# Performance work log

Hardware: AMD Instinct MI355X
Metric: run time of the kernel (lower is better)

## Reference

```python
import jax, jax.numpy as jnp
import numpy as np

N_NODES = 100000
N_EDGES = 1600000
IN_DIM = 128
HID = 64
N_CLASSES = 40
NEG_SLOPE = 0.2


def setup_inputs() -> dict:
    key = jax.random.key(0)
    ks = jax.random.split(key, 12)
    s_in = 1.0 / np.sqrt(IN_DIM)
    s_h = 1.0 / np.sqrt(HID)
    return {
        "x": jax.random.normal(ks[0], (N_NODES, IN_DIM), dtype=jnp.float32),
        "edge_index": jax.random.randint(ks[1], (2, N_EDGES), 0, N_NODES, dtype=jnp.int64),
        "W0": jax.random.normal(ks[2], (IN_DIM, HID), dtype=jnp.float32) * s_in,
        "a_s0": jax.random.normal(ks[3], (HID,), dtype=jnp.float32) * s_h,
        "a_d0": jax.random.normal(ks[4], (HID,), dtype=jnp.float32) * s_h,
        "b0": jnp.zeros((HID,), dtype=jnp.float32),
        "W1": jax.random.normal(ks[5], (HID, HID), dtype=jnp.float32) * s_h,
        "a_s1": jax.random.normal(ks[6], (HID,), dtype=jnp.float32) * s_h,
        "a_d1": jax.random.normal(ks[7], (HID,), dtype=jnp.float32) * s_h,
        "b1": jnp.zeros((HID,), dtype=jnp.float32),
        "Wl": jax.random.normal(ks[8], (HID, N_CLASSES), dtype=jnp.float32) * s_h,
        "bl": jnp.zeros((N_CLASSES,), dtype=jnp.float32),
    }


def gat_conv(x, src, dst, W, a_s, a_d, b, n_nodes):
    # single-head GATConv (PyG default heads=1), self-loops already in src/dst
    h = x @ W                                  # [N, d]
    e = jax.nn.leaky_relu((h @ a_s)[src] + (h @ a_d)[dst], NEG_SLOPE)  # [E]
    # segment softmax over incoming edges of each dst node
    m = jax.ops.segment_max(e, dst, num_segments=n_nodes)
    p = jnp.exp(e - m[dst])
    denom = jax.ops.segment_sum(p, dst, num_segments=n_nodes)
    alpha = p / (denom[dst] + 1e-16)           # [E]
    out = jax.ops.segment_sum(alpha[:, None] * h[src], dst, num_segments=n_nodes)
    return out + b


def reference(x, edge_index, W0, a_s0, a_d0, b0, W1, a_s1, a_d1, b1, Wl, bl):
    n = x.shape[0]
    loop = jnp.arange(n, dtype=edge_index.dtype)
    src = jnp.concatenate([edge_index[0], loop])
    dst = jnp.concatenate([edge_index[1], loop])
    h = gat_conv(x, src, dst, W0, a_s0, a_d0, b0, n)
    h = jax.nn.elu(h)
    h = gat_conv(h, src, dst, W1, a_s1, a_d1, b1, n)
    h = jax.nn.elu(h)
    return h @ Wl + bl
```

## Files before the change

### kernel.cpp

```cpp
#include <hip/hip_runtime.h>
#include <math.h>

#define NEG_SLOPE 0.2f
#define CAP 256
#define BSH 9
#define BSZ 512
#define CHUNK 4096
#define PADS 16
#define CAPQ 16384
#define CAPB 10240

typedef __attribute__((ext_vector_type(8))) short short8;
typedef __attribute__((ext_vector_type(4))) float f32x4;

__device__ __forceinline__ float hred_sum(float v) {
#pragma unroll
    for (int o = 16; o >= 1; o >>= 1) v += __shfl_xor(v, o, 64);
    return v;
}
__device__ __forceinline__ unsigned int f2bf(float f) {
    unsigned int u = __float_as_uint(f);
    return (u + 0x7fffu + ((u >> 16) & 1u)) >> 16;
}
__device__ __forceinline__ float bflo(unsigned int u) { return __uint_as_float(u << 16); }
__device__ __forceinline__ float bfhi(unsigned int u) { return __uint_as_float(u & 0xffff0000u); }


__device__ __forceinline__ void scatter_body(char* smem, int bid,
        const int* __restrict__ src, const int* __restrict__ dst,
        int* __restrict__ bcursor, int* __restrict__ ebuf, int E) {
    int* lh = (int*)smem;
    int* lb = lh + 256;
    const int tid = threadIdx.x;
    int base = bid * CHUNK;
    int sv[16], dv[16];
    bool ok[16];
#pragma unroll
    for (int u = 0; u < 16; ++u) {
        int i = base + u * 256 + tid;
        ok[u] = i < E;
        int ii = ok[u] ? i : E - 1;
        dv[u] = dst[ii];
        sv[u] = src[ii];
    }
    lh[tid] = 0;
    __syncthreads();
#pragma unroll
    for (int u = 0; u < 16; ++u)
        if (ok[u]) atomicAdd(&lh[dv[u] >> BSH], 1);
    __syncthreads();
    int c = lh[tid];
    lb[tid] = c ? atomicAdd(&bcursor[tid * PADS], c) : 0;
    lh[tid] = 0;
    __syncthreads();
#pragma unroll
    for (int u = 0; u < 16; ++u) {
        if (ok[u]) {
            int d = dv[u], b = d >> BSH;
            int pp = atomicAdd(&lh[b], 1);
            int pos = lb[b] + pp;
            if (pos < CAPQ)
                ebuf[b * CAPQ + pos] = (sv[u] << BSH) | (d & (BSZ - 1));
        }
    }
}

__device__ __forceinline__ void gemm0_body(char* smem, int bid,
        const float* __restrict__ X, const float* __restrict__ W,
        const float* __restrict__ a_s, const float* __restrict__ a_d,
        unsigned int* __restrict__ hb, float* __restrict__ ss, float* __restrict__ sd, int N) {
    constexpr int K = 128, OUTW = 64, NKC = K / 32, NC = OUTW / 16;
    short* wfrag = (short*)smem;
    unsigned int* hs = (unsigned int*)(smem + NKC * NC * 64 * 8 * 2);

    const int tid  = threadIdx.x;
    const int lane = tid & 63;
    const int w    = tid >> 6;
    const int m    = lane & 15;
    const int q8   = lane >> 4;
    const int rowbase = bid * 64 + w * 16;

    for (int f = tid; f < NKC * NC * 64; f += 256) {
        int flane = f & 63;
        int fc    = (f >> 6) % NC;
        int fkc   = (f >> 6) / NC;
        int col   = fc * 16 + (flane & 15);
        int k0    = fkc * 32 + (flane >> 4) * 8;
        short8 b;
#pragma unroll
        for (int j = 0; j < 8; ++j) b[j] = (short)f2bf(W[(k0 + j) * OUTW + col]);
        *(short8*)&wfrag[f * 8] = b;
    }
    __syncthreads();

    int grow = rowbase + m; if (grow >= N) grow = N - 1;

    f32x4 acc[NC];
#pragma unroll
    for (int c = 0; c < NC; ++c) acc[c] = (f32x4)0.f;

    const float* xrow = X + (size_t)grow * K + q8 * 8;
#pragma unroll
    for (int kc = 0; kc < NKC; ++kc) {
        float4 v0 = *(const float4*)(xrow + kc * 32);
        float4 v1 = *(const float4*)(xrow + kc * 32 + 4);
        float vv[8] = {v0.x, v0.y, v0.z, v0.w, v1.x, v1.y, v1.z, v1.w};
        short8 ah, al;
#pragma unroll
        for (int j = 0; j < 8; ++j) {
            unsigned int hb16 = f2bf(vv[j]);
            ah[j] = (short)hb16;
            al[j] = (short)f2bf(vv[j] - __uint_as_float(hb16 << 16));
        }
#pragma unroll
        for (int c = 0; c < NC; ++c) {
            short8 b = *(short8*)&wfrag[((kc * NC + c) * 64 + lane) * 8];
            acc[c] = __builtin_amdgcn_mfma_f32_16x16x32_bf16(ah, b, acc[c], 0, 0, 0);
            acc[c] = __builtin_amdgcn_mfma_f32_16x16x32_bf16(al, b, acc[c], 0, 0, 0);
        }
    }

    float asv[NC], adv[NC];
#pragma unroll
    for (int c = 0; c < NC; ++c) { asv[c] = a_s[c * 16 + m]; adv[c] = a_d[c * 16 + m]; }
#pragma unroll
    for (int i = 0; i < 4; ++i) {
        float s = 0.f, d = 0.f;
#pragma unroll
        for (int c = 0; c < NC; ++c) {
            s = fmaf(acc[c][i], asv[c], s);
            d = fmaf(acc[c][i], adv[c], d);
        }
#pragma unroll
        for (int o = 1; o <= 8; o <<= 1) {
            s += __shfl_xor(s, o, 64);
            d += __shfl_xor(d, o, 64);
        }
        int r = rowbase + q8 * 4 + i;
        if (m == 0 && r < N) { ss[r] = s; sd[r] = d; }
    }

    unsigned short* hsw = (unsigned short*)&hs[w * 512];
#pragma unroll
    for (int c = 0; c < NC; ++c)
#pragma unroll
        for (int i = 0; i < 4; ++i)
            hsw[(q8 * 4 + i) * 64 + c * 16 + m] = (unsigned short)f2bf(acc[c][i]);
    unsigned int* hu = &hs[w * 512];
    int row = lane >> 2, u0 = (lane & 3) * 8;
    uint4 va = *(uint4*)&hu[row * 32 + u0];
    uint4 vb = *(uint4*)&hu[row * 32 + u0 + 4];
    int r = rowbase + row;
    if (r < N) {
        *(uint4*)&hb[(size_t)r * 32 + u0]     = va;
        *(uint4*)&hb[(size_t)r * 32 + u0 + 4] = vb;
    }
}

__global__ __launch_bounds__(256) void k_scatter_gemm0(
        const int* __restrict__ src, const int* __restrict__ dst,
        int* __restrict__ bcursor, int* __restrict__ ebuf, int E, int nscat,
        const float* __restrict__ X, const float* __restrict__ W,
        const float* __restrict__ a_s, const float* __restrict__ a_d,
        unsigned int* __restrict__ hb, float* __restrict__ ss, float* __restrict__ sd, int N) {
    __shared__ __align__(16) char smem[24576];
    if ((int)blockIdx.x < nscat)
        scatter_body(smem, blockIdx.x, src, dst, bcursor, ebuf, E);
    else
        gemm0_body(smem, blockIdx.x - nscat, X, W, a_s, a_d, hb, ss, sd, N);
}


__global__ __launch_bounds__(256) void k_cscan(const int* __restrict__ bcursor,
                                               int* __restrict__ boff, int* __restrict__ ecnt,
                                               int* __restrict__ rowptr, int nbuck, int N) {
    __shared__ int s2[256];
    int t = threadIdx.x;
    int bc = 0;
    if (t < nbuck) { bc = bcursor[t * PADS]; if (bc > CAPQ) bc = CAPQ; }
    int cn = 0;
    if (t < nbuck) { cn = N - (t << BSH); if (cn > BSZ) cn = BSZ; if (cn < 0) cn = 0; }
    int tot = bc + cn;
    s2[t] = tot;
    __syncthreads();
#pragma unroll
    for (int off = 1; off < 256; off <<= 1) {
        int u = (t >= off) ? s2[t - off] : 0;
        __syncthreads();
        s2[t] += u;
        __syncthreads();
    }
    if (t < nbuck) { boff[t] = s2[t] - tot; ecnt[t] = bc; }
    if (t == 255) rowptr[N] = s2[255];
}


__global__ __launch_bounds__(1024) void k_build(const int* __restrict__ boff,
                                                const int* __restrict__ ecnt, const int* __restrict__ ebuf,
                                                int* __restrict__ rowptr, int* __restrict__ csr, int N) {
    __shared__ int sdeg[BSZ], sscan[BSZ];
    __shared__ int sebuf[CAPB];
    int b = blockIdx.x, t = threadIdx.x;
    int nlo = b << BSH;
    int cn = N - nlo; if (cn > BSZ) cn = BSZ;
    int e0 = b * CAPQ, ec = ecnt[b], cb = boff[b];
    if (t < BSZ) sdeg[t] = (t < cn) ? 1 : 0;
    __syncthreads();
    int ecl = ec < CAPB ? ec : CAPB;
    {
        int i = t;
        for (; i + 3 * 1024 < ecl; i += 4 * 1024) {
            int r0 = ebuf[e0 + i],        r1 = ebuf[e0 + i + 1024];
            int r2 = ebuf[e0 + i + 2048], r3 = ebuf[e0 + i + 3072];
            sebuf[i] = r0; sebuf[i + 1024] = r1; sebuf[i + 2048] = r2; sebuf[i + 3072] = r3;
            atomicAdd(&sdeg[r0 & (BSZ - 1)], 1);
            atomicAdd(&sdeg[r1 & (BSZ - 1)], 1);
            atomicAdd(&sdeg[r2 & (BSZ - 1)], 1);
            atomicAdd(&sdeg[r3 & (BSZ - 1)], 1);
        }
        for (; i < ecl; i += 1024) {
            int r = ebuf[e0 + i];
            sebuf[i] = r;
            atomicAdd(&sdeg[r & (BSZ - 1)], 1);
        }
        for (i = CAPB + t; i < ec; i += 1024)
            atomicAdd(&sdeg[ebuf[e0 + i] & (BSZ - 1)], 1);
    }
    __syncthreads();
    int v = 0;
    if (t < BSZ) { v = sdeg[t]; sscan[t] = v; }
    __syncthreads();
#pragma unroll
    for (int off = 1; off < BSZ; off <<= 1) {
        int u = 0;
        if (t < BSZ && t >= off) u = sscan[t - off];
        __syncthreads();
        if (t < BSZ) sscan[t] += u;
        __syncthreads();
    }
    if (t < BSZ) {
        int excl = sscan[t] - v;
        if (t < cn) {
            rowptr[nlo + t] = cb + excl;
            csr[cb + excl] = nlo + t;
            sdeg[t] = excl + 1;
        }
    }
    __syncthreads();
    {
        int i = t;
        for (; i + 3 * 1024 < ecl; i += 4 * 1024) {
            int r0 = sebuf[i],        r1 = sebuf[i + 1024];
            int r2 = sebuf[i + 2048], r3 = sebuf[i + 3072];
            int p0 = atomicAdd(&sdeg[r0 & (BSZ - 1)], 1);
            int p1 = atomicAdd(&sdeg[r1 & (BSZ - 1)], 1);
            int p2 = atomicAdd(&sdeg[r2 & (BSZ - 1)], 1);
            int p3 = atomicAdd(&sdeg[r3 & (BSZ - 1)], 1);
            csr[cb + p0] = r0 >> BSH;
            csr[cb + p1] = r1 >> BSH;
            csr[cb + p2] = r2 >> BSH;
            csr[cb + p3] = r3 >> BSH;
        }
        for (; i < ecl; i += 1024) {
            int rec = sebuf[i];
            int p = atomicAdd(&sdeg[rec & (BSZ - 1)], 1);
            csr[cb + p] = rec >> BSH;
        }
        for (i = CAPB + t; i < ec; i += 1024) {
            int rec = ebuf[e0 + i];
            int p = atomicAdd(&sdeg[rec & (BSZ - 1)], 1);
            csr[cb + p] = rec >> BSH;
        }
    }
}


template <int K, int OUTW, bool SS, bool HB, bool XB>
__global__ __launch_bounds__(256) void k_gemm(const void* __restrict__ X,
                                              const float* __restrict__ W,
                                              const float* __restrict__ a_s,
                                              const float* __restrict__ a_d,
                                              const float* __restrict__ bias,
                                              void* __restrict__ Hout,
                                              float* __restrict__ ss,
                                              float* __restrict__ sd, int N) {
    constexpr int NKC = K / 32;
    constexpr int NC  = (OUTW + 15) / 16;
    __shared__ __align__(16) short wfrag[NKC * NC * 64 * 8];
    __shared__ __align__(16) unsigned int hs[HB ? 4 : 1][16 * 32];

    const int tid  = threadIdx.x;
    const int lane = tid & 63;
    const int w    = tid >> 6;
    const int m    = lane & 15;
    const int q8   = lane >> 4;
    const int rowbase = blockIdx.x * 64 + w * 16;

    for (int f = tid; f < NKC * NC * 64; f += 256) {
        int flane = f & 63;
        int fc    = (f >> 6) % NC;
        int fkc   = (f >> 6) / NC;
        int col   = fc * 16 + (flane & 15);
        int k0    = fkc * 32 + (flane >> 4) * 8;
        short8 b;
#pragma unroll
        for (int j = 0; j < 8; ++j) {
            float v = (col < OUTW) ? W[(k0 + j) * OUTW + col] : 0.f;
            b[j] = (short)f2bf(v);
        }
        *(short8*)&wfrag[f * 8] = b;
    }
    __syncthreads();

    int grow = rowbase + m; if (grow >= N) grow = N - 1;

    f32x4 acc[NC];
#pragma unroll
    for (int c = 0; c < NC; ++c) acc[c] = (f32x4)0.f;

    if (XB) {
        const unsigned short* xrow = (const unsigned short*)X + (size_t)grow * 64 + q8 * 8;
#pragma unroll
        for (int kc = 0; kc < NKC; ++kc) {
            short8 ah = *(const short8*)(xrow + kc * 32);
#pragma unroll
            for (int c = 0; c < NC; ++c) {
                short8 b = *(short8*)&wfrag[((kc * NC + c) * 64 + lane) * 8];
                acc[c] = __builtin_amdgcn_mfma_f32_16x16x32_bf16(ah, b, acc[c], 0, 0, 0);
            }
        }
    } else {
        const float* xrow = (const float*)X + (size_t)grow * K + q8 * 8;
#pragma unroll
        for (int kc = 0; kc < NKC; ++kc) {
            float4 v0 = *(const float4*)(xrow + kc * 32);
            float4 v1 = *(const float4*)(xrow + kc * 32 + 4);
            float vv[8] = {v0.x, v0.y, v0.z, v0.w, v1.x, v1.y, v1.z, v1.w};
            short8 ah, al;
#pragma unroll
            for (int j = 0; j < 8; ++j) {
                unsigned int hb16 = f2bf(vv[j]);
                ah[j] = (short)hb16;
                al[j] = (short)f2bf(vv[j] - __uint_as_float(hb16 << 16));
            }
#pragma unroll
            for (int c = 0; c < NC; ++c) {
                short8 b = *(short8*)&wfrag[((kc * NC + c) * 64 + lane) * 8];
                acc[c] = __builtin_amdgcn_mfma_f32_16x16x32_bf16(ah, b, acc[c], 0, 0, 0);
                acc[c] = __builtin_amdgcn_mfma_f32_16x16x32_bf16(al, b, acc[c], 0, 0, 0);
            }
        }
    }

    if (SS) {
        float asv[NC], adv[NC];
#pragma unroll
        for (int c = 0; c < NC; ++c) { asv[c] = a_s[c * 16 + m]; adv[c] = a_d[c * 16 + m]; }
#pragma unroll
        for (int i = 0; i < 4; ++i) {
            float s = 0.f, d = 0.f;
#pragma unroll
            for (int c = 0; c < NC; ++c) {
                s = fmaf(acc[c][i], asv[c], s);
                d = fmaf(acc[c][i], adv[c], d);
            }
#pragma unroll
            for (int o = 1; o <= 8; o <<= 1) {
                s += __shfl_xor(s, o, 64);
                d += __shfl_xor(d, o, 64);
            }
            int r = rowbase + q8 * 4 + i;
            if (m == 0 && r < N) { ss[r] = s; sd[r] = d; }
        }
    }

    if (HB) {
        unsigned short* hsw = (unsigned short*)&hs[w][0];
#pragma unroll
        for (int c = 0; c < NC; ++c)
#pragma unroll
            for (int i = 0; i < 4; ++i)
                hsw[(q8 * 4 + i) * 64 + c * 16 + m] = (unsigned short)f2bf(acc[c][i]);
        unsigned int* hu = &hs[w][0];
        int row = lane >> 2, u0 = (lane & 3) * 8;
        uint4 va = *(uint4*)&hu[row * 32 + u0];
        uint4 vb = *(uint4*)&hu[row * 32 + u0 + 4];
        int r = rowbase + row;
        if (r < N) {
            unsigned int* hbp = (unsigned int*)Hout;
            *(uint4*)&hbp[(size_t)r * 32 + u0]     = va;
            *(uint4*)&hbp[(size_t)r * 32 + u0 + 4] = vb;
        }
    } else {
        float bv[NC];
#pragma unroll
        for (int c = 0; c < NC; ++c) {
            int col = c * 16 + m;
            bv[c] = (col < OUTW) ? bias[col] : 0.f;
        }
        float* O = (float*)Hout;
#pragma unroll
        for (int i = 0; i < 4; ++i) {
            int r = rowbase + q8 * 4 + i;
            if (r < N) {
#pragma unroll
                for (int c = 0; c < NC; ++c) {
                    int col = c * 16 + m;
                    if (col < OUTW) O[(size_t)r * OUTW + col] = acc[c][i] + bv[c];
                }
            }
        }
    }
}


__global__ __launch_bounds__(256) void k_agg(const int* __restrict__ rowptr, const int* __restrict__ csr,
                                             const float* __restrict__ ss, const float* __restrict__ sd,
                                             const unsigned int* __restrict__ hb, const float* __restrict__ bias,
                                             unsigned int* __restrict__ z, int N) {
    __shared__ __align__(16) float sal[8][CAP];
    __shared__ __align__(16) int   sof[8][CAP];
    const int tid = threadIdx.x;
    const int hw  = tid >> 5;
    const int p   = tid & 31;
    const int n   = blockIdx.x * 8 + hw;
    const bool valid = n < N;
    const char* hbb = (const char*)hb;
    const int p4 = p * 4;

    int ro = 0, deg = 0;
    float sdn = 0.f;
    if (valid) {
        ro  = rowptr[n];
        deg = rowptr[n + 1] - ro;
        sdn = sd[n];
    }

    if (deg <= CAP) {
        float sum = 0.f;
        for (int j = p; j < deg; j += 32) {
            int s = csr[ro + j];
            float e = ss[s] + sdn;
            e = fmaxf(e, NEG_SLOPE * e);
            float pe = __expf(e);
            sal[hw][j] = pe;
            sof[hw][j] = s << 7;
            sum += pe;
        }
        sum = hred_sum(sum);
        float inv = 1.f / (sum + 1e-16f);

        float ax = 0.f, ay = 0.f, bx = 0.f, by = 0.f, cx = 0.f, cy = 0.f, dx = 0.f, dy = 0.f;
        int j = 0;
        for (; j + 7 < deg; j += 8) {
            float4 al0 = *(const float4*)&sal[hw][j];
            float4 al1 = *(const float4*)&sal[hw][j + 4];
            int4   of0 = *(const int4*)&sof[hw][j];
            int4   of1 = *(const int4*)&sof[hw][j + 4];
            unsigned int u0 = *(const unsigned int*)(hbb + (of0.x + p4));
            unsigned int u1 = *(const unsigned int*)(hbb + (of0.y + p4));
            unsigned int u2 = *(const unsigned int*)(hbb + (of0.z + p4));
            unsigned int u3 = *(const unsigned int*)(hbb + (of0.w + p4));
            unsigned int u4 = *(const unsigned int*)(hbb + (of1.x + p4));
            unsigned int u5 = *(const unsigned int*)(hbb + (of1.y + p4));
            unsigned int u6 = *(const unsigned int*)(hbb + (of1.z + p4));
            unsigned int u7 = *(const unsigned int*)(hbb + (of1.w + p4));
            ax = fmaf(bflo(u0), al0.x, ax); ay = fmaf(bfhi(u0), al0.x, ay);
            bx = fmaf(bflo(u1), al0.y, bx); by = fmaf(bfhi(u1), al0.y, by);
            cx = fmaf(bflo(u2), al0.z, cx); cy = fmaf(bfhi(u2), al0.z, cy);
            dx = fmaf(bflo(u3), al0.w, dx); dy = fmaf(bfhi(u3), al0.w, dy);
            ax = fmaf(bflo(u4), al1.x, ax); ay = fmaf(bfhi(u4), al1.x, ay);
            bx = fmaf(bflo(u5), al1.y, bx); by = fmaf(bfhi(u5), al1.y, by);
            cx = fmaf(bflo(u6), al1.z, cx); cy = fmaf(bfhi(u6), al1.z, cy);
            dx = fmaf(bflo(u7), al1.w, dx); dy = fmaf(bfhi(u7), al1.w, dy);
        }
        for (; j + 3 < deg; j += 4) {
            float4 al0 = *(const float4*)&sal[hw][j];
            int4   of0 = *(const int4*)&sof[hw][j];
            unsigned int u0 = *(const unsigned int*)(hbb + (of0.x + p4));
            unsigned int u1 = *(const unsigned int*)(hbb + (of0.y + p4));
            unsigned int u2 = *(const unsigned int*)(hbb + (of0.z + p4));
            unsigned int u3 = *(const unsigned int*)(hbb + (of0.w + p4));
            ax = fmaf(bflo(u0), al0.x, ax); ay = fmaf(bfhi(u0), al0.x, ay);
            bx = fmaf(bflo(u1), al0.y, bx); by = fmaf(bfhi(u1), al0.y, by);
            cx = fmaf(bflo(u2), al0.z, cx); cy = fmaf(bfhi(u2), al0.z, cy);
            dx = fmaf(bflo(u3), al0.w, dx); dy = fmaf(bfhi(u3), al0.w, dy);
        }
        for (; j < deg; ++j) {
            float a = sal[hw][j];
            unsigned int u0 = *(const unsigned int*)(hbb + (sof[hw][j] + p4));
            ax = fmaf(bflo(u0), a, ax); ay = fmaf(bfhi(u0), a, ay);
        }
        float fx = (ax + bx) + (cx + dx);
        float fy = (ay + by) + (cy + dy);
        if (valid) {
            float2 ob = *(const float2*)&bias[p * 2];
            float ox = fmaf(fx, inv, ob.x);
            float oy = fmaf(fy, inv, ob.y);
            ox = (ox > 0.f) ? ox : __expf(ox) - 1.f;
            oy = (oy > 0.f) ? oy : __expf(oy) - 1.f;
            z[(size_t)n * 32 + p] = (f2bf(oy) << 16) | f2bf(ox);
        }
    } else {
        float sum = 0.f;
        for (int j = p; j < deg; j += 32) {
            int s = csr[ro + j];
            float e = ss[s] + sdn;
            e = fmaxf(e, NEG_SLOPE * e);
            sum += __expf(e);
        }
        sum = hred_sum(sum);
        float inv = 1.f / (sum + 1e-16f);
        float fx = 0.f, fy = 0.f;
        for (int j = 0; j < deg; ++j) {
            int s = csr[ro + j];
            float e = ss[s] + sdn;
            e = fmaxf(e, NEG_SLOPE * e);
            float pe = __expf(e);
            unsigned int u = *(const unsigned int*)(hbb + ((s << 7) + p4));
            fx = fmaf(bflo(u), pe, fx); fy = fmaf(bfhi(u), pe, fy);
        }
        float2 ob = *(const float2*)&bias[p * 2];
        float ox = fmaf(fx, inv, ob.x);
        float oy = fmaf(fy, inv, ob.y);
        ox = (ox > 0.f) ? ox : __expf(ox) - 1.f;
        oy = (oy > 0.f) ? oy : __expf(oy) - 1.f;
        z[(size_t)n * 32 + p] = (f2bf(oy) << 16) | f2bf(ox);
    }
}


extern "C" void kernel_launch(void* const* d_in, const int* in_sizes, int n_in,
                              void* d_out, int out_size, void* d_ws, size_t ws_size,
                              hipStream_t stream) {
    const float* x   = (const float*)d_in[0];
    const int*   ei  = (const int*)d_in[1];
    const float* W0  = (const float*)d_in[2];
    const float* as0 = (const float*)d_in[3];
    const float* ad0 = (const float*)d_in[4];
    const float* b0  = (const float*)d_in[5];
    const float* W1  = (const float*)d_in[6];
    const float* as1 = (const float*)d_in[7];
    const float* ad1 = (const float*)d_in[8];
    const float* b1  = (const float*)d_in[9];
    const float* Wl  = (const float*)d_in[10];
    const float* bl  = (const float*)d_in[11];
    float* out = (float*)d_out;

    int N = in_sizes[0] / 128;
    int E = in_sizes[1] / 2;
    const int* srcp = ei;
    const int* dstp = ei + E;
    int nbuck = (N + BSZ - 1) >> BSH;

    char* wp = (char*)d_ws;
    auto alloc = [&](size_t bytes) { void* p = (void*)wp; wp += (bytes + 255) & ~(size_t)255; return p; };
    unsigned int* hb = (unsigned int*)alloc((size_t)N * 32 * 4);
    unsigned int* z  = (unsigned int*)alloc((size_t)N * 32 * 4);
    float* ssb     = (float*)alloc((size_t)N * 4);
    float* sdb     = (float*)alloc((size_t)N * 4);
    int*   rowptr  = (int*)alloc((size_t)(N + 1) * 4);
    int*   csr     = (int*)alloc((size_t)(E + N) * 4);
    int*   ebuf    = (int*)alloc((size_t)nbuck * CAPQ * 4);
    int*   boff    = (int*)alloc(256 * 4);
    int*   ecnt    = (int*)alloc(256 * 4);
    int*   bcursor = (int*)alloc(256 * PADS * 4);

    int nscat = (E + CHUNK - 1) / CHUNK;
    int gb = (N + 63) / 64;

    hipMemsetAsync(bcursor, 0, 256 * PADS * 4, stream);
    k_scatter_gemm0<<<nscat + gb, 256, 0, stream>>>(srcp, dstp, bcursor, ebuf, E, nscat,
                                                    x, W0, as0, ad0, hb, ssb, sdb, N);
    k_cscan<<<1, 256, 0, stream>>>(bcursor, boff, ecnt, rowptr, nbuck, N);
    k_build<<<nbuck, 1024, 0, stream>>>(boff, ecnt, ebuf, rowptr, csr, N);

    k_agg<<<(N + 7) / 8, 256, 0, stream>>>(rowptr, csr, ssb, sdb, hb, b0, z, N);
    k_gemm<64, 64, true, true, true><<<gb, 256, 0, stream>>>(z, W1, as1, ad1, nullptr, hb, ssb, sdb, N);
    k_agg<<<(N + 7) / 8, 256, 0, stream>>>(rowptr, csr, ssb, sdb, hb, b1, z, N);
    k_gemm<64, 40, false, false, true><<<gb, 256, 0, stream>>>(z, Wl, nullptr, nullptr, bl, out, nullptr, nullptr, N);
}
```

Measured before the change: 243.5 us.

## Fold bucket scan into CSR build and single-pass aggregation without LDS staging

The single-block bucket prefix-scan kernel is removed. Each k_build block now redoes the 256-entry scan in shared memory and takes its own offset, which saves one launch and one dependent step. k_agg drops the two-phase LDS staging of attention weights and offsets. Each half-wave now walks the neighbor list once, with every lane redundantly loading the csr indices and ss values and computing exp, so the softmax sum and the weighted feature sum accumulate together. This removes the LDS round trip, shuffles and barriers, but adds redundant scalar loads and exp work per lane.

```diff
diff --git a/kernel.cpp b/kernel.cpp
--- a/kernel.cpp
+++ b/kernel.cpp
@@ -2,7 +2,6 @@
 #include <math.h>
 
 #define NEG_SLOPE 0.2f
-#define CAP 256
 #define BSH 9
 #define BSZ 512
 #define CHUNK 4096
@@ -13,11 +12,6 @@
 typedef __attribute__((ext_vector_type(8))) short short8;
 typedef __attribute__((ext_vector_type(4))) float f32x4;
 
-__device__ __forceinline__ float hred_sum(float v) {
-#pragma unroll
-    for (int o = 16; o >= 1; o >>= 1) v += __shfl_xor(v, o, 64);
-    return v;
-}
 __device__ __forceinline__ unsigned int f2bf(float f) {
     unsigned int u = __float_as_uint(f);
     return (u + 0x7fffu + ((u >> 16) & 1u)) >> 16;
@@ -171,39 +165,42 @@
 }
 
 
-__global__ __launch_bounds__(256) void k_cscan(const int* __restrict__ bcursor,
-                                               int* __restrict__ boff, int* __restrict__ ecnt,
-                                               int* __restrict__ rowptr, int nbuck, int N) {
-    __shared__ int s2[256];
-    int t = threadIdx.x;
-    int bc = 0;
-    if (t < nbuck) { bc = bcursor[t * PADS]; if (bc > CAPQ) bc = CAPQ; }
-    int cn = 0;
-    if (t < nbuck) { cn = N - (t << BSH); if (cn > BSZ) cn = BSZ; if (cn < 0) cn = 0; }
-    int tot = bc + cn;
-    s2[t] = tot;
-    __syncthreads();
-#pragma unroll
-    for (int off = 1; off < 256; off <<= 1) {
-        int u = (t >= off) ? s2[t - off] : 0;
-        __syncthreads();
-        s2[t] += u;
-        __syncthreads();
-    }
-    if (t < nbuck) { boff[t] = s2[t] - tot; ecnt[t] = bc; }
-    if (t == 255) rowptr[N] = s2[255];
-}
-
-
-__global__ __launch_bounds__(1024) void k_build(const int* __restrict__ boff,
-                                                const int* __restrict__ ecnt, const int* __restrict__ ebuf,
-                                                int* __restrict__ rowptr, int* __restrict__ csr, int N) {
+__global__ __launch_bounds__(1024) void k_build(const int* __restrict__ bcursor,
+                                                const int* __restrict__ ebuf,
+                                                int* __restrict__ rowptr, int* __restrict__ csr,
+                                                int N, int nbuck) {
     __shared__ int sdeg[BSZ], sscan[BSZ];
     __shared__ int sebuf[CAPB];
+    __shared__ int shdr[2];
     int b = blockIdx.x, t = threadIdx.x;
     int nlo = b << BSH;
     int cn = N - nlo; if (cn > BSZ) cn = BSZ;
-    int e0 = b * CAPQ, ec = ecnt[b], cb = boff[b];
+
+    int bcv = 0, totv = 0;
+    if (t < 256) {
+        int cnb = 0;
+        if (t < nbuck) {
+            bcv = bcursor[t * PADS]; if (bcv > CAPQ) bcv = CAPQ;
+            cnb = N - (t << BSH); if (cnb > BSZ) cnb = BSZ; if (cnb < 0) cnb = 0;
+        }
+        totv = bcv + cnb;
+        sscan[t] = totv;
+    }
+    __syncthreads();
+#pragma unroll
+    for (int off = 1; off < 256; off <<= 1) {
+        int u = 0;
+        if (t < 256 && t >= off) u = sscan[t - off];
+        __syncthreads();
+        if (t < 256) sscan[t] += u;
+        __syncthreads();
+    }
+    if (t == b) { shdr[0] = sscan[t] - totv; shdr[1] = bcv; }
+    if (b == 0 && t == nbuck - 1) rowptr[N] = sscan[t];
+    __syncthreads();
+    int cb = shdr[0], ec = shdr[1];
+    int e0 = b * CAPQ;
+
     if (t < BSZ) sdeg[t] = (t < cn) ? 1 : 0;
     __syncthreads();
     int ecl = ec < CAPB ? ec : CAPB;
@@ -418,15 +415,11 @@
                                              const float* __restrict__ ss, const float* __restrict__ sd,
                                              const unsigned int* __restrict__ hb, const float* __restrict__ bias,
                                              unsigned int* __restrict__ z, int N) {
-    __shared__ __align__(16) float sal[8][CAP];
-    __shared__ __align__(16) int   sof[8][CAP];
     const int tid = threadIdx.x;
     const int hw  = tid >> 5;
     const int p   = tid & 31;
     const int n   = blockIdx.x * 8 + hw;
     const bool valid = n < N;
-    const char* hbb = (const char*)hb;
-    const int p4 = p * 4;
 
     int ro = 0, deg = 0;
     float sdn = 0.f;
@@ -436,90 +429,76 @@
         sdn = sd[n];
     }
 
-    if (deg <= CAP) {
-        float sum = 0.f;
-        for (int j = p; j < deg; j += 32) {
-            int s = csr[ro + j];
-            float e = ss[s] + sdn;
-            e = fmaxf(e, NEG_SLOPE * e);
-            float pe = __expf(e);
-            sal[hw][j] = pe;
-            sof[hw][j] = s << 7;
-            sum += pe;
-        }
-        sum = hred_sum(sum);
+    float fx0 = 0.f, fy0 = 0.f, fx1 = 0.f, fy1 = 0.f;
+    float fx2 = 0.f, fy2 = 0.f, fx3 = 0.f, fy3 = 0.f;
+    float sum0 = 0.f, sum1 = 0.f;
+
+    int j = 0;
+    for (; j + 7 < deg; j += 8) {
+        int s0 = csr[ro + j],     s1 = csr[ro + j + 1];
+        int s2 = csr[ro + j + 2], s3 = csr[ro + j + 3];
+        int s4 = csr[ro + j + 4], s5 = csr[ro + j + 5];
+        int s6 = csr[ro + j + 6], s7 = csr[ro + j + 7];
+        unsigned int u0 = hb[(unsigned)s0 * 32 + p];
+        unsigned int u1 = hb[(unsigned)s1 * 32 + p];
+        unsigned int u2 = hb[(unsigned)s2 * 32 + p];
+        unsigned int u3 = hb[(unsigned)s3 * 32 + p];
+        unsigned int u4 = hb[(unsigned)s4 * 32 + p];
+        unsigned int u5 = hb[(unsigned)s5 * 32 + p];
+        unsigned int u6 = hb[(unsigned)s6 * 32 + p];
+        unsigned int u7 = hb[(unsigned)s7 * 32 + p];
+        float e0 = ss[s0] + sdn, e1 = ss[s1] + sdn, e2 = ss[s2] + sdn, e3 = ss[s3] + sdn;
+        float e4 = ss[s4] + sdn, e5 = ss[s5] + sdn, e6 = ss[s6] + sdn, e7 = ss[s7] + sdn;
+        e0 = fmaxf(e0, NEG_SLOPE * e0); e1 = fmaxf(e1, NEG_SLOPE * e1);
+        e2 = fmaxf(e2, NEG_SLOPE * e2); e3 = fmaxf(e3, NEG_SLOPE * e3);
+        e4 = fmaxf(e4, NEG_SLOPE * e4); e5 = fmaxf(e5, NEG_SLOPE * e5);
+        e6 = fmaxf(e6, NEG_SLOPE * e6); e7 = fmaxf(e7, NEG_SLOPE * e7);
+        float p0 = __expf(e0), p1 = __expf(e1), p2 = __expf(e2), p3 = __expf(e3);
+        float p4 = __expf(e4), p5 = __expf(e5), p6 = __expf(e6), p7 = __expf(e7);
+        sum0 += (p0 + p2) + (p4 + p6);
+        sum1 += (p1 + p3) + (p5 + p7);
+        fx0 = fmaf(bflo(u0), p0, fx0); fy0 = fmaf(bfhi(u0), p0, fy0);
+        fx1 = fmaf(bflo(u1), p1, fx1); fy1 = fmaf(bfhi(u1), p1, fy1);
+        fx2 = fmaf(bflo(u2), p2, fx2); fy2 = fmaf(bfhi(u2), p2, fy2);
+        fx3 = fmaf(bflo(u3), p3, fx3); fy3 = fmaf(bfhi(u3), p3, fy3);
+        fx0 = fmaf(bflo(u4), p4, fx0); fy0 = fmaf(bfhi(u4), p4, fy0);
+        fx1 = fmaf(bflo(u5), p5, fx1); fy1 = fmaf(bfhi(u5), p5, fy1);
+        fx2 = fmaf(bflo(u6), p6, fx2); fy2 = fmaf(bfhi(u6), p6, fy2);
+        fx3 = fmaf(bflo(u7), p7, fx3); fy3 = fmaf(bfhi(u7), p7, fy3);
+    }
+    for (; j + 3 < deg; j += 4) {
+        int s0 = csr[ro + j],     s1 = csr[ro + j + 1];
+        int s2 = csr[ro + j + 2], s3 = csr[ro + j + 3];
+        unsigned int u0 = hb[(unsigned)s0 * 32 + p];
+        unsigned int u1 = hb[(unsigned)s1 * 32 + p];
+        unsigned int u2 = hb[(unsigned)s2 * 32 + p];
+        unsigned int u3 = hb[(unsigned)s3 * 32 + p];
+        float e0 = ss[s0] + sdn, e1 = ss[s1] + sdn, e2 = ss[s2] + sdn, e3 = ss[s3] + sdn;
+        e0 = fmaxf(e0, NEG_SLOPE * e0); e1 = fmaxf(e1, NEG_SLOPE * e1);
+        e2 = fmaxf(e2, NEG_SLOPE * e2); e3 = fmaxf(e3, NEG_SLOPE * e3);
+        float p0 = __expf(e0), p1 = __expf(e1), p2 = __expf(e2), p3 = __expf(e3);
+        sum0 += p0 + p2;
+        sum1 += p1 + p3;
+        fx0 = fmaf(bflo(u0), p0, fx0); fy0 = fmaf(bfhi(u0), p0, fy0);
+        fx1 = fmaf(bflo(u1), p1, fx1); fy1 = fmaf(bfhi(u1), p1, fy1);
+        fx2 = fmaf(bflo(u2), p2, fx2); fy2 = fmaf(bfhi(u2), p2, fy2);
+        fx3 = fmaf(bflo(u3), p3, fx3); fy3 = fmaf(bfhi(u3), p3, fy3);
+    }
+    for (; j < deg; ++j) {
+        int s0 = csr[ro + j];
+        unsigned int u0 = hb[(unsigned)s0 * 32 + p];
+        float e0 = ss[s0] + sdn;
+        e0 = fmaxf(e0, NEG_SLOPE * e0);
+        float p0 = __expf(e0);
+        sum0 += p0;
+        fx0 = fmaf(bflo(u0), p0, fx0); fy0 = fmaf(bfhi(u0), p0, fy0);
+    }
+
+    if (valid) {
+        float sum = sum0 + sum1;
         float inv = 1.f / (sum + 1e-16f);
-
-        float ax = 0.f, ay = 0.f, bx = 0.f, by = 0.f, cx = 0.f, cy = 0.f, dx = 0.f, dy = 0.f;
-        int j = 0;
-        for (; j + 7 < deg; j += 8) {
-            float4 al0 = *(const float4*)&sal[hw][j];
-            float4 al1 = *(const float4*)&sal[hw][j + 4];
-            int4   of0 = *(const int4*)&sof[hw][j];
-            int4   of1 = *(const int4*)&sof[hw][j + 4];
-            unsigned int u0 = *(const unsigned int*)(hbb + (of0.x + p4));
-            unsigned int u1 = *(const unsigned int*)(hbb + (of0.y + p4));
-            unsigned int u2 = *(const unsigned int*)(hbb + (of0.z + p4));
-            unsigned int u3 = *(const unsigned int*)(hbb + (of0.w + p4));
-            unsigned int u4 = *(const unsigned int*)(hbb + (of1.x + p4));
-            unsigned int u5 = *(const unsigned int*)(hbb + (of1.y + p4));
-            unsigned int u6 = *(const unsigned int*)(hbb + (of1.z + p4));
-            unsigned int u7 = *(const unsigned int*)(hbb + (of1.w + p4));
-            ax = fmaf(bflo(u0), al0.x, ax); ay = fmaf(bfhi(u0), al0.x, ay);
-            bx = fmaf(bflo(u1), al0.y, bx); by = fmaf(bfhi(u1), al0.y, by);
-            cx = fmaf(bflo(u2), al0.z, cx); cy = fmaf(bfhi(u2), al0.z, cy);
-            dx = fmaf(bflo(u3), al0.w, dx); dy = fmaf(bfhi(u3), al0.w, dy);
-            ax = fmaf(bflo(u4), al1.x, ax); ay = fmaf(bfhi(u4), al1.x, ay);
-            bx = fmaf(bflo(u5), al1.y, bx); by = fmaf(bfhi(u5), al1.y, by);
-            cx = fmaf(bflo(u6), al1.z, cx); cy = fmaf(bfhi(u6), al1.z, cy);
-            dx = fmaf(bflo(u7), al1.w, dx); dy = fmaf(bfhi(u7), al1.w, dy);
-        }
-        for (; j + 3 < deg; j += 4) {
-            float4 al0 = *(const float4*)&sal[hw][j];
-            int4   of0 = *(const int4*)&sof[hw][j];
-            unsigned int u0 = *(const unsigned int*)(hbb + (of0.x + p4));
-            unsigned int u1 = *(const unsigned int*)(hbb + (of0.y + p4));
-            unsigned int u2 = *(const unsigned int*)(hbb + (of0.z + p4));
-            unsigned int u3 = *(const unsigned int*)(hbb + (of0.w + p4));
-            ax = fmaf(bflo(u0), al0.x, ax); ay = fmaf(bfhi(u0), al0.x, ay);
-            bx = fmaf(bflo(u1), al0.y, bx); by = fmaf(bfhi(u1), al0.y, by);
-            cx = fmaf(bflo(u2), al0.z, cx); cy = fmaf(bfhi(u2), al0.z, cy);
-            dx = fmaf(bflo(u3), al0.w, dx); dy = fmaf(bfhi(u3), al0.w, dy);
-        }
-        for (; j < deg; ++j) {
-            float a = sal[hw][j];
-            unsigned int u0 = *(const unsigned int*)(hbb + (sof[hw][j] + p4));
-            ax = fmaf(bflo(u0), a, ax); ay = fmaf(bfhi(u0), a, ay);
-        }
-        float fx = (ax + bx) + (cx + dx);
-        float fy = (ay + by) + (cy + dy);
-        if (valid) {
-            float2 ob = *(const float2*)&bias[p * 2];
-            float ox = fmaf(fx, inv, ob.x);
-            float oy = fmaf(fy, inv, ob.y);
-            ox = (ox > 0.f) ? ox : __expf(ox) - 1.f;
-            oy = (oy > 0.f) ? oy : __expf(oy) - 1.f;
-            z[(size_t)n * 32 + p] = (f2bf(oy) << 16) | f2bf(ox);
-        }
-    } else {
-        float sum = 0.f;
-        for (int j = p; j < deg; j += 32) {
-            int s = csr[ro + j];
-            float e = ss[s] + sdn;
-            e = fmaxf(e, NEG_SLOPE * e);
-            sum += __expf(e);
-        }
-        sum = hred_sum(sum);
-        float inv = 1.f / (sum + 1e-16f);
-        float fx = 0.f, fy = 0.f;
-        for (int j = 0; j < deg; ++j) {
-            int s = csr[ro + j];
-            float e = ss[s] + sdn;
-            e = fmaxf(e, NEG_SLOPE * e);
-            float pe = __expf(e);
-            unsigned int u = *(const unsigned int*)(hbb + ((s << 7) + p4));
-            fx = fmaf(bflo(u), pe, fx); fy = fmaf(bfhi(u), pe, fy);
-        }
+        float fx = (fx0 + fx1) + (fx2 + fx3);
+        float fy = (fy0 + fy1) + (fy2 + fy3);
         float2 ob = *(const float2*)&bias[p * 2];
         float ox = fmaf(fx, inv, ob.x);
         float oy = fmaf(fy, inv, ob.y);
@@ -562,8 +541,6 @@
     int*   rowptr  = (int*)alloc((size_t)(N + 1) * 4);
     int*   csr     = (int*)alloc((size_t)(E + N) * 4);
     int*   ebuf    = (int*)alloc((size_t)nbuck * CAPQ * 4);
-    int*   boff    = (int*)alloc(256 * 4);
-    int*   ecnt    = (int*)alloc(256 * 4);
     int*   bcursor = (int*)alloc(256 * PADS * 4);
 
     int nscat = (E + CHUNK - 1) / CHUNK;
@@ -572,8 +549,7 @@
     hipMemsetAsync(bcursor, 0, 256 * PADS * 4, stream);
     k_scatter_gemm0<<<nscat + gb, 256, 0, stream>>>(srcp, dstp, bcursor, ebuf, E, nscat,
                                                     x, W0, as0, ad0, hb, ssb, sdb, N);
-    k_cscan<<<1, 256, 0, stream>>>(bcursor, boff, ecnt, rowptr, nbuck, N);
-    k_build<<<nbuck, 1024, 0, stream>>>(boff, ecnt, ebuf, rowptr, csr, N);
+    k_build<<<nbuck, 1024, 0, stream>>>(bcursor, ebuf, rowptr, csr, N, nbuck);
 
     k_agg<<<(N + 7) / 8, 256, 0, stream>>>(rowptr, csr, ssb, sdb, hb, b0, z, N);
     k_gemm<64, 64, true, true, true><<<gb, 256, 0, stream>>>(z, W1, as1, ad1, nullptr, hb, ssb, sdb, N);
```

After: 254.0 us. 4.3% more time.
